# Kernel optimization log

Hardware: AMD Instinct MI355X
Metric: run time of the kernel (lower is better)

Reference implementation:

```python
import jax, jax.numpy as jnp
import numpy as np

H = 5  # hidden size == input size

def setup_inputs() -> dict:
    key = jax.random.key(0)
    ks = jax.random.split(key, 12)
    B, T = 8192, 512
    s = 1.0 / np.sqrt(H)
    x = jax.random.normal(ks[0], (B, T, H), dtype=jnp.float32)
    # LSTM params (PyTorch layout: [4H, in], gate order i,f,g,o)
    W_ih = jax.random.uniform(ks[1], (4 * H, H), jnp.float32, -s, s)
    W_hh = jax.random.uniform(ks[2], (4 * H, H), jnp.float32, -s, s)
    b_ih = jax.random.uniform(ks[3], (4 * H,), jnp.float32, -s, s)
    b_hh = jax.random.uniform(ks[4], (4 * H,), jnp.float32, -s, s)
    # MLP head 5->32->32->5 (PyTorch Linear layout: [out, in])
    W1 = jax.random.uniform(ks[5], (32, H), jnp.float32, -s, s)
    b1 = jax.random.uniform(ks[6], (32,), jnp.float32, -s, s)
    s2 = 1.0 / np.sqrt(32)
    W2 = jax.random.uniform(ks[7], (32, 32), jnp.float32, -s2, s2)
    b2 = jax.random.uniform(ks[8], (32,), jnp.float32, -s2, s2)
    W3 = jax.random.uniform(ks[9], (H, 32), jnp.float32, -s2, s2)
    b3 = jax.random.uniform(ks[10], (H,), jnp.float32, -s2, s2)
    return {"x": x, "W_ih": W_ih, "W_hh": W_hh, "b_ih": b_ih, "b_hh": b_hh,
            "W1": W1, "b1": b1, "W2": W2, "b2": b2, "W3": W3, "b3": b3}


def _lstm_last_hidden(x, W_ih, W_hh, b_ih, b_hh):
    # x: [B, T, H]. Precompute input projections for all steps: [T, B, 4H]
    xz = jnp.einsum('bth,gh->tbg', x, W_ih) + (b_ih + b_hh)
    B = x.shape[0]
    h0 = jnp.zeros((B, H), x.dtype)
    c0 = jnp.zeros((B, H), x.dtype)

    def step(carry, z_t):
        h, c = carry
        z = z_t + h @ W_hh.T  # [B, 4H]
        i = jax.nn.sigmoid(z[:, 0:H])
        f = jax.nn.sigmoid(z[:, H:2 * H])
        g = jnp.tanh(z[:, 2 * H:3 * H])
        o = jax.nn.sigmoid(z[:, 3 * H:4 * H])
        c = f * c + i * g
        h = o * jnp.tanh(c)
        return (h, c), None

    (h, _), _ = jax.lax.scan(step, (h0, c0), xz)
    return h  # [B, H]


def reference(x, W_ih, W_hh, b_ih, b_hh, W1, b1, W2, b2, W3, b3):
    h_last = _lstm_last_hidden(x, W_ih, W_hh, b_ih, b_hh)
    out = h_last + x[:, -1, :]                # residual with last input step
    out = jax.nn.relu(out @ W1.T + b1)
    out = jax.nn.relu(out @ W2.T + b2)
    out = out @ W3.T + b3
    return out
```

## Files before the change

kernel.cpp:

```cpp
#include <hip/hip_runtime.h>


#define LOG2E 1.44269504088896f

__device__ __forceinline__ float hexp2(float x) { return __builtin_amdgcn_exp2f(x); }
__device__ __forceinline__ float hrcp(float x)  { return __builtin_amdgcn_rcpf(x); }

template<int CTRL>
__device__ __forceinline__ float dpp_mov(float x) {
  int r = __builtin_amdgcn_update_dpp(0, __builtin_bit_cast(int, x),
                                      CTRL, 0xF, 0xF, true);
  return __builtin_bit_cast(float, r);
}
template<int CTRL, int BANKMASK>
__device__ __forceinline__ float dpp_merge(float old, float src) {
  int r = __builtin_amdgcn_update_dpp(__builtin_bit_cast(int, old),
                                      __builtin_bit_cast(int, src),
                                      CTRL, 0xF, BANKMASK, false);
  return __builtin_bit_cast(float, r);
}

constexpr int TT   = 512;
constexpr int HD   = 5;
constexpr int RPB  = 8;
constexpr int CHNK = 32;
constexpr int RSTR = 164;
constexpr int XOFF = RPB * RSTR;
constexpr int NCH  = TT / CHNK;

__global__ __launch_bounds__(64, 1) void lstm_mlp_kernel(
    const float* __restrict__ x,   const float* __restrict__ Wih,
    const float* __restrict__ Whh, const float* __restrict__ bih,
    const float* __restrict__ bhh, const float* __restrict__ W1,
    const float* __restrict__ b1,  const float* __restrict__ W2,
    const float* __restrict__ b2,  const float* __restrict__ W3,
    const float* __restrict__ b3,  float* __restrict__ out, int B)
{
  const int lane = threadIdx.x;
  const int grp  = lane >> 3;
  const int j    = lane & 7;
  const int jj   = (j < 5) ? j : 0;
  const int blockRow = blockIdx.x * RPB;
  const int row  = blockRow + grp;
  const bool act = (j < 5) && (row < B);

  __shared__ float xbuf[2 * XOFF];
  __shared__ float sh[RPB][5];
  __shared__ float s1[RPB][32];
  __shared__ float s2[RPB][32];

  float wih[4][5], whh[4][5], bsum[4];
#pragma unroll
  for (int G = 0; G < 4; ++G) {
    const float sc = (G == 2) ? (2.0f * LOG2E) : (-LOG2E);
#pragma unroll
    for (int k = 0; k < 5; ++k) {
      wih[G][k] = Wih[(G * 5 + jj) * 5 + k] * sc;
      whh[G][k] = Whh[(G * 5 + jj) * 5 + k] * sc;
    }
    bsum[G] = (bih[G * 5 + jj] + bhh[G * 5 + jj]) * sc;
  }

  const int rowc = (row < B) ? row : (B - 1);
  const float xlast = x[(size_t)rowc * (TT * HD) + 511 * HD + jj];

  const float4* gp[5];
  int wa[5];
#pragma unroll
  for (int i = 0; i < 5; ++i) {
    int u  = i * 64 + lane;
    int r  = u / 40;
    int o4 = u - r * 40;
    int gr = blockRow + r; if (gr >= B) gr = B - 1;
    gp[i]  = (const float4*)(x + (size_t)gr * (TT * HD)) + o4;
    wa[i]  = r * RSTR + o4 * 4;
  }

  float4 st0, st1, st2, st3, st4;
  st0 = *gp[0]; gp[0] += 40; st1 = *gp[1]; gp[1] += 40;
  st2 = *gp[2]; gp[2] += 40; st3 = *gp[3]; gp[3] += 40;
  st4 = *gp[4]; gp[4] += 40;
  *(float4*)&xbuf[wa[0]] = st0; *(float4*)&xbuf[wa[1]] = st1;
  *(float4*)&xbuf[wa[2]] = st2; *(float4*)&xbuf[wa[3]] = st3;
  *(float4*)&xbuf[wa[4]] = st4;
  st0 = *gp[0]; gp[0] += 40; st1 = *gp[1]; gp[1] += 40;
  st2 = *gp[2]; gp[2] += 40; st3 = *gp[3]; gp[3] += 40;
  st4 = *gp[4]; gp[4] += 40;

  float c = 0.0f;
  float hv0 = 0.f, hv1 = 0.f, hv2 = 0.f, hv3 = 0.f, hv4 = 0.f;

  auto step = [&](float x0, float x1, float x2, float x3, float x4) {
    float z[4];
#pragma unroll
    for (int G = 0; G < 4; ++G) {
      float a = bsum[G];
      a = fmaf(x0, wih[G][0], a);
      a = fmaf(x1, wih[G][1], a);
      a = fmaf(x2, wih[G][2], a);
      a = fmaf(x3, wih[G][3], a);
      a = fmaf(x4, wih[G][4], a);
      a = fmaf(hv0, whh[G][0], a);
      a = fmaf(hv1, whh[G][1], a);
      a = fmaf(hv2, whh[G][2], a);
      a = fmaf(hv3, whh[G][3], a);
      a = fmaf(hv4, whh[G][4], a);
      z[G] = a;
    }
    float ig = hrcp(1.0f + hexp2(z[0]));
    float fg = hrcp(1.0f + hexp2(z[1]));
    float gv = fmaf(-2.0f, hrcp(1.0f + hexp2(z[2])), 1.0f);
    float og = hrcp(1.0f + hexp2(z[3]));
    c = fmaf(fg, c, ig * gv);
    float th = fmaf(-2.0f, hrcp(1.0f + hexp2(c * (2.0f * LOG2E))), 1.0f);
    float h  = og * th;
    float q0 = dpp_mov<0x00>(h);
    float q1 = dpp_mov<0x55>(h);
    float q2 = dpp_mov<0xAA>(h);
    float q3 = dpp_mov<0xFF>(h);
    hv0 = dpp_merge<0x114, 0xA>(q0, q0);
    hv1 = dpp_merge<0x114, 0xA>(q1, q1);
    hv2 = dpp_merge<0x114, 0xA>(q2, q2);
    hv3 = dpp_merge<0x114, 0xA>(q3, q3);
    hv4 = dpp_merge<0x104, 0x5>(q0, q0);
  };

  auto step4 = [&](float4 A, float4 Bv, float4 C, float4 D, float4 E) {
    step(A.x, A.y, A.z, A.w, Bv.x);
    step(Bv.y, Bv.z, Bv.w, C.x, C.y);
    step(C.z, C.w, D.x, D.y, D.z);
    step(D.w, E.x, E.y, E.z, E.w);
  };

  auto rdg = [&](int fi, float4& A, float4& Bv, float4& C, float4& D, float4& E) {
    const float4* p = (const float4*)&xbuf[fi];
    A = p[0]; Bv = p[1]; C = p[2]; D = p[3]; E = p[4];
  };

  float4 A0, A1, A2, A3, A4;
  float4 B0, B1, B2, B3, B4;

#pragma unroll 1
  for (int ch = 0; ch < NCH; ++ch) {
    const int bo_cur  = (ch & 1) ? XOFF : 0;
    const int bo_next = XOFF - bo_cur;
    if (ch < NCH - 1) {
      *(float4*)&xbuf[wa[0] + bo_next] = st0;
      *(float4*)&xbuf[wa[1] + bo_next] = st1;
      *(float4*)&xbuf[wa[2] + bo_next] = st2;
      *(float4*)&xbuf[wa[3] + bo_next] = st3;
      *(float4*)&xbuf[wa[4] + bo_next] = st4;
    }
    if (ch < NCH - 2) {
      st0 = *gp[0]; gp[0] += 40; st1 = *gp[1]; gp[1] += 40;
      st2 = *gp[2]; gp[2] += 40; st3 = *gp[3]; gp[3] += 40;
      st4 = *gp[4]; gp[4] += 40;
    }
    const int xb = bo_cur + grp * RSTR;
    rdg(xb +   0, A0, A1, A2, A3, A4);
    rdg(xb +  20, B0, B1, B2, B3, B4);
    step4(A0, A1, A2, A3, A4); rdg(xb +  40, A0, A1, A2, A3, A4);
    step4(B0, B1, B2, B3, B4); rdg(xb +  60, B0, B1, B2, B3, B4);
    step4(A0, A1, A2, A3, A4); rdg(xb +  80, A0, A1, A2, A3, A4);
    step4(B0, B1, B2, B3, B4); rdg(xb + 100, B0, B1, B2, B3, B4);
    step4(A0, A1, A2, A3, A4); rdg(xb + 120, A0, A1, A2, A3, A4);
    step4(B0, B1, B2, B3, B4); rdg(xb + 140, B0, B1, B2, B3, B4);
    step4(A0, A1, A2, A3, A4);
    step4(B0, B1, B2, B3, B4);
  }

  if (j < 5) sh[grp][j] = hv4 * 0.0f + (hv0 * 0.0f) + 0.0f +
                          ((j == 0) ? hv0 : (j == 1) ? hv1 : (j == 2) ? hv2 :
                           (j == 3) ? hv3 : hv4) + xlast;
  float in5_0 = sh[grp][0], in5_1 = sh[grp][1], in5_2 = sh[grp][2],
        in5_3 = sh[grp][3], in5_4 = sh[grp][4];

#pragma unroll
  for (int p = 0; p < 4; ++p) {
    int m = p * 8 + j;
    float acc = b1[m];
    acc = fmaf(W1[m * 5 + 0], in5_0, acc);
    acc = fmaf(W1[m * 5 + 1], in5_1, acc);
    acc = fmaf(W1[m * 5 + 2], in5_2, acc);
    acc = fmaf(W1[m * 5 + 3], in5_3, acc);
    acc = fmaf(W1[m * 5 + 4], in5_4, acc);
    s1[grp][m] = fmaxf(acc, 0.0f);
  }
  float y1[32];
#pragma unroll
  for (int k = 0; k < 32; ++k) y1[k] = s1[grp][k];

  auto dot32 = [&](const float* W, int m, const float* y, float b) {
    float acc = b;
    const float4* w4 = (const float4*)(W + m * 32);
#pragma unroll
    for (int k4 = 0; k4 < 8; ++k4) {
      float4 w = w4[k4];
      acc = fmaf(w.x, y[k4 * 4 + 0], acc);
      acc = fmaf(w.y, y[k4 * 4 + 1], acc);
      acc = fmaf(w.z, y[k4 * 4 + 2], acc);
      acc = fmaf(w.w, y[k4 * 4 + 3], acc);
    }
    return acc;
  };

#pragma unroll
  for (int p = 0; p < 4; ++p) {
    int m = p * 8 + j;
    s2[grp][m] = fmaxf(dot32(W2, m, y1, b2[m]), 0.0f);
  }
  float y2[32];
#pragma unroll
  for (int k = 0; k < 32; ++k) y2[k] = s2[grp][k];

  if (act) out[row * HD + j] = dot32(W3, j, y2, b3[j]);
}

extern "C" void kernel_launch(void* const* d_in, const int* in_sizes, int n_in,
                              void* d_out, int out_size, void* d_ws, size_t ws_size,
                              hipStream_t stream) {
  const float* x   = (const float*)d_in[0];
  const float* Wih = (const float*)d_in[1];
  const float* Whh = (const float*)d_in[2];
  const float* bih = (const float*)d_in[3];
  const float* bhh = (const float*)d_in[4];
  const float* W1  = (const float*)d_in[5];
  const float* b1  = (const float*)d_in[6];
  const float* W2  = (const float*)d_in[7];
  const float* b2  = (const float*)d_in[8];
  const float* W3  = (const float*)d_in[9];
  const float* b3  = (const float*)d_in[10];

  int B = in_sizes[0] / (TT * HD);
  int grid = (B + RPB - 1) / RPB;
  hipLaunchKernelGGL(lstm_mlp_kernel, dim3(grid), dim3(64), 0, stream,
                     x, Wih, Whh, bih, bhh, W1, b1, W2, b2, W3, b3,
                     (float*)d_out, B);
}
```

Before: 206.7 us.

## Split LSTM into producer wave for input projections and consumer wave for recurrence

The block grows to two waves. One wave streams x into LDS and computes the input-gate projections (W_ih·x + bias) into a double-buffered LDS window. The other wave reads those precomputed projections and runs only the W_hh recurrence plus the MLP head, with block barriers handing each window across. The aim is to take the input-projection FMAs and the global-load staging off the serial recurrence wave. The cost is extra LDS traffic, per-window barriers and twice the threads per block.

```diff
diff --git a/kernel.cpp b/kernel.cpp
--- a/kernel.cpp
+++ b/kernel.cpp
@@ -27,8 +27,14 @@
 constexpr int RSTR = 164;
 constexpr int XOFF = RPB * RSTR;
 constexpr int NCH  = TT / CHNK;
-
-__global__ __launch_bounds__(64, 1) void lstm_mlp_kernel(
+constexpr int WST  = 16;
+constexpr int ZSTR = 20;
+constexpr int ZROW = RPB * ZSTR;
+constexpr int ZWIN = WST * ZROW;
+
+__global__ __attribute__((amdgpu_flat_work_group_size(128, 128),
+                          amdgpu_waves_per_eu(2, 2)))
+void lstm_mlp_kernel(
     const float* __restrict__ x,   const float* __restrict__ Wih,
     const float* __restrict__ Whh, const float* __restrict__ bih,
     const float* __restrict__ bhh, const float* __restrict__ W1,
@@ -36,70 +42,155 @@
     const float* __restrict__ b2,  const float* __restrict__ W3,
     const float* __restrict__ b3,  float* __restrict__ out, int B)
 {
-  const int lane = threadIdx.x;
+  const int tid  = threadIdx.x;
+  const int wid  = tid >> 6;
+  const int lane = tid & 63;
   const int grp  = lane >> 3;
   const int j    = lane & 7;
   const int jj   = (j < 5) ? j : 0;
   const int blockRow = blockIdx.x * RPB;
   const int row  = blockRow + grp;
-  const bool act = (j < 5) && (row < B);
-
-  __shared__ float xbuf[2 * XOFF];
-  __shared__ float sh[RPB][5];
+
+  __shared__ __align__(16) float xbuf[2 * XOFF];
+  __shared__ __align__(16) float zbuf[2 * ZWIN];
   __shared__ float s1[RPB][32];
   __shared__ float s2[RPB][32];
 
-  float wih[4][5], whh[4][5], bsum[4];
+  if (wid == 1) {
+    float wih[4][5], bsum[4];
+#pragma unroll
+    for (int G = 0; G < 4; ++G) {
+      const float sc = (G == 2) ? (2.0f * LOG2E) : (-LOG2E);
+#pragma unroll
+      for (int k = 0; k < 5; ++k)
+        wih[G][k] = Wih[(G * 5 + jj) * 5 + k] * sc;
+      bsum[G] = (bih[G * 5 + jj] + bhh[G * 5 + jj]) * sc;
+    }
+
+    const float4* gp[5];
+    int wa[5];
+#pragma unroll
+    for (int i = 0; i < 5; ++i) {
+      int u  = i * 64 + lane;
+      int r  = u / 40;
+      int o4 = u - r * 40;
+      int gr = blockRow + r; if (gr >= B) gr = B - 1;
+      gp[i]  = (const float4*)(x + (size_t)gr * (TT * HD)) + o4;
+      wa[i]  = r * RSTR + o4 * 4;
+    }
+
+    float4 st0, st1, st2, st3, st4;
+    st0 = *gp[0]; gp[0] += 40; st1 = *gp[1]; gp[1] += 40;
+    st2 = *gp[2]; gp[2] += 40; st3 = *gp[3]; gp[3] += 40;
+    st4 = *gp[4]; gp[4] += 40;
+    *(float4*)&xbuf[wa[0]] = st0; *(float4*)&xbuf[wa[1]] = st1;
+    *(float4*)&xbuf[wa[2]] = st2; *(float4*)&xbuf[wa[3]] = st3;
+    *(float4*)&xbuf[wa[4]] = st4;
+    st0 = *gp[0]; gp[0] += 40; st1 = *gp[1]; gp[1] += 40;
+    st2 = *gp[2]; gp[2] += 40; st3 = *gp[3]; gp[3] += 40;
+    st4 = *gp[4]; gp[4] += 40;
+
+    float* zb = zbuf + grp * ZSTR + jj * 4;
+
+    auto prodstep = [&](float x0, float x1, float x2, float x3, float x4,
+                        float* zp) {
+      float a[4];
+#pragma unroll
+      for (int G = 0; G < 4; ++G) {
+        float a0 = bsum[G];
+        a0 = fmaf(x0, wih[G][0], a0);
+        a0 = fmaf(x1, wih[G][1], a0);
+        a0 = fmaf(x2, wih[G][2], a0);
+        a0 = fmaf(x3, wih[G][3], a0);
+        a0 = fmaf(x4, wih[G][4], a0);
+        a[G] = a0;
+      }
+      if (j < 5) {
+        float4 v; v.x = a[0]; v.y = a[1]; v.z = a[2]; v.w = a[3];
+        *(float4*)zp = v;
+      }
+    };
+    auto prod4 = [&](float4 A, float4 Bv, float4 C, float4 D, float4 E,
+                     float* zp) {
+      prodstep(A.x, A.y, A.z, A.w, Bv.x, zp);
+      prodstep(Bv.y, Bv.z, Bv.w, C.x, C.y, zp + 1 * ZROW);
+      prodstep(C.z, C.w, D.x, D.y, D.z, zp + 2 * ZROW);
+      prodstep(D.w, E.x, E.y, E.z, E.w, zp + 3 * ZROW);
+    };
+    auto rdg = [&](int fi, float4& A, float4& Bv, float4& C, float4& D, float4& E) {
+      const float4* p = (const float4*)&xbuf[fi];
+      A = p[0]; Bv = p[1]; C = p[2]; D = p[3]; E = p[4];
+    };
+
+    float4 A0, A1, A2, A3, A4;
+    float4 B0, B1, B2, B3, B4;
+
+#pragma unroll 1
+    for (int ch = 0; ch < NCH; ++ch) {
+      const int bo_cur  = (ch & 1) ? XOFF : 0;
+      const int bo_next = XOFF - bo_cur;
+      if (ch < NCH - 1) {
+        *(float4*)&xbuf[wa[0] + bo_next] = st0;
+        *(float4*)&xbuf[wa[1] + bo_next] = st1;
+        *(float4*)&xbuf[wa[2] + bo_next] = st2;
+        *(float4*)&xbuf[wa[3] + bo_next] = st3;
+        *(float4*)&xbuf[wa[4] + bo_next] = st4;
+      }
+      if (ch < NCH - 2) {
+        st0 = *gp[0]; gp[0] += 40; st1 = *gp[1]; gp[1] += 40;
+        st2 = *gp[2]; gp[2] += 40; st3 = *gp[3]; gp[3] += 40;
+        st4 = *gp[4]; gp[4] += 40;
+      }
+      const int xb = bo_cur + grp * RSTR;
+
+      rdg(xb +  0, A0, A1, A2, A3, A4);
+      rdg(xb + 20, B0, B1, B2, B3, B4);
+      prod4(A0, A1, A2, A3, A4, zb + 0 * ZROW);
+      rdg(xb + 40, A0, A1, A2, A3, A4);
+      prod4(B0, B1, B2, B3, B4, zb + 4 * ZROW);
+      rdg(xb + 60, B0, B1, B2, B3, B4);
+      prod4(A0, A1, A2, A3, A4, zb +  8 * ZROW);
+      prod4(B0, B1, B2, B3, B4, zb + 12 * ZROW);
+      __syncthreads();
+
+      float* z1 = zb + ZWIN;
+      rdg(xb +  80, A0, A1, A2, A3, A4);
+      rdg(xb + 100, B0, B1, B2, B3, B4);
+      prod4(A0, A1, A2, A3, A4, z1 + 0 * ZROW);
+      rdg(xb + 120, A0, A1, A2, A3, A4);
+      prod4(B0, B1, B2, B3, B4, z1 + 4 * ZROW);
+      rdg(xb + 140, B0, B1, B2, B3, B4);
+      prod4(A0, A1, A2, A3, A4, z1 +  8 * ZROW);
+      prod4(B0, B1, B2, B3, B4, z1 + 12 * ZROW);
+      __syncthreads();
+    }
+    return;
+  }
+
+  float whh[4][5];
 #pragma unroll
   for (int G = 0; G < 4; ++G) {
     const float sc = (G == 2) ? (2.0f * LOG2E) : (-LOG2E);
 #pragma unroll
-    for (int k = 0; k < 5; ++k) {
-      wih[G][k] = Wih[(G * 5 + jj) * 5 + k] * sc;
+    for (int k = 0; k < 5; ++k)
       whh[G][k] = Whh[(G * 5 + jj) * 5 + k] * sc;
-    }
-    bsum[G] = (bih[G * 5 + jj] + bhh[G * 5 + jj]) * sc;
   }
 
   const int rowc = (row < B) ? row : (B - 1);
-  const float xlast = x[(size_t)rowc * (TT * HD) + 511 * HD + jj];
-
-  const float4* gp[5];
-  int wa[5];
-#pragma unroll
-  for (int i = 0; i < 5; ++i) {
-    int u  = i * 64 + lane;
-    int r  = u / 40;
-    int o4 = u - r * 40;
-    int gr = blockRow + r; if (gr >= B) gr = B - 1;
-    gp[i]  = (const float4*)(x + (size_t)gr * (TT * HD)) + o4;
-    wa[i]  = r * RSTR + o4 * 4;
-  }
-
-  float4 st0, st1, st2, st3, st4;
-  st0 = *gp[0]; gp[0] += 40; st1 = *gp[1]; gp[1] += 40;
-  st2 = *gp[2]; gp[2] += 40; st3 = *gp[3]; gp[3] += 40;
-  st4 = *gp[4]; gp[4] += 40;
-  *(float4*)&xbuf[wa[0]] = st0; *(float4*)&xbuf[wa[1]] = st1;
-  *(float4*)&xbuf[wa[2]] = st2; *(float4*)&xbuf[wa[3]] = st3;
-  *(float4*)&xbuf[wa[4]] = st4;
-  st0 = *gp[0]; gp[0] += 40; st1 = *gp[1]; gp[1] += 40;
-  st2 = *gp[2]; gp[2] += 40; st3 = *gp[3]; gp[3] += 40;
-  st4 = *gp[4]; gp[4] += 40;
+  const float xl0 = x[(size_t)rowc * (TT * HD) + 511 * HD + 0];
+  const float xl1 = x[(size_t)rowc * (TT * HD) + 511 * HD + 1];
+  const float xl2 = x[(size_t)rowc * (TT * HD) + 511 * HD + 2];
+  const float xl3 = x[(size_t)rowc * (TT * HD) + 511 * HD + 3];
+  const float xl4 = x[(size_t)rowc * (TT * HD) + 511 * HD + 4];
 
   float c = 0.0f;
   float hv0 = 0.f, hv1 = 0.f, hv2 = 0.f, hv3 = 0.f, hv4 = 0.f;
 
-  auto step = [&](float x0, float x1, float x2, float x3, float x4) {
-    float z[4];
+  auto stepz = [&](float4 zn) {
+    float z[4] = {zn.x, zn.y, zn.z, zn.w};
 #pragma unroll
     for (int G = 0; G < 4; ++G) {
-      float a = bsum[G];
-      a = fmaf(x0, wih[G][0], a);
-      a = fmaf(x1, wih[G][1], a);
-      a = fmaf(x2, wih[G][2], a);
-      a = fmaf(x3, wih[G][3], a);
-      a = fmaf(x4, wih[G][4], a);
+      float a = z[G];
       a = fmaf(hv0, whh[G][0], a);
       a = fmaf(hv1, whh[G][1], a);
       a = fmaf(hv2, whh[G][2], a);
@@ -125,55 +216,23 @@
     hv4 = dpp_merge<0x104, 0x5>(q0, q0);
   };
 
-  auto step4 = [&](float4 A, float4 Bv, float4 C, float4 D, float4 E) {
-    step(A.x, A.y, A.z, A.w, Bv.x);
-    step(Bv.y, Bv.z, Bv.w, C.x, C.y);
-    step(C.z, C.w, D.x, D.y, D.z);
-    step(D.w, E.x, E.y, E.z, E.w);
-  };
-
-  auto rdg = [&](int fi, float4& A, float4& Bv, float4& C, float4& D, float4& E) {
-    const float4* p = (const float4*)&xbuf[fi];
-    A = p[0]; Bv = p[1]; C = p[2]; D = p[3]; E = p[4];
-  };
-
-  float4 A0, A1, A2, A3, A4;
-  float4 B0, B1, B2, B3, B4;
-
 #pragma unroll 1
-  for (int ch = 0; ch < NCH; ++ch) {
-    const int bo_cur  = (ch & 1) ? XOFF : 0;
-    const int bo_next = XOFF - bo_cur;
-    if (ch < NCH - 1) {
-      *(float4*)&xbuf[wa[0] + bo_next] = st0;
-      *(float4*)&xbuf[wa[1] + bo_next] = st1;
-      *(float4*)&xbuf[wa[2] + bo_next] = st2;
-      *(float4*)&xbuf[wa[3] + bo_next] = st3;
-      *(float4*)&xbuf[wa[4] + bo_next] = st4;
-    }
-    if (ch < NCH - 2) {
-      st0 = *gp[0]; gp[0] += 40; st1 = *gp[1]; gp[1] += 40;
-      st2 = *gp[2]; gp[2] += 40; st3 = *gp[3]; gp[3] += 40;
-      st4 = *gp[4]; gp[4] += 40;
-    }
-    const int xb = bo_cur + grp * RSTR;
-    rdg(xb +   0, A0, A1, A2, A3, A4);
-    rdg(xb +  20, B0, B1, B2, B3, B4);
-    step4(A0, A1, A2, A3, A4); rdg(xb +  40, A0, A1, A2, A3, A4);
-    step4(B0, B1, B2, B3, B4); rdg(xb +  60, B0, B1, B2, B3, B4);
-    step4(A0, A1, A2, A3, A4); rdg(xb +  80, A0, A1, A2, A3, A4);
-    step4(B0, B1, B2, B3, B4); rdg(xb + 100, B0, B1, B2, B3, B4);
-    step4(A0, A1, A2, A3, A4); rdg(xb + 120, A0, A1, A2, A3, A4);
-    step4(B0, B1, B2, B3, B4); rdg(xb + 140, B0, B1, B2, B3, B4);
-    step4(A0, A1, A2, A3, A4);
-    step4(B0, B1, B2, B3, B4);
-  }
-
-  if (j < 5) sh[grp][j] = hv4 * 0.0f + (hv0 * 0.0f) + 0.0f +
-                          ((j == 0) ? hv0 : (j == 1) ? hv1 : (j == 2) ? hv2 :
-                           (j == 3) ? hv3 : hv4) + xlast;
-  float in5_0 = sh[grp][0], in5_1 = sh[grp][1], in5_2 = sh[grp][2],
-        in5_3 = sh[grp][3], in5_4 = sh[grp][4];
+  for (int w = 0; w < 2 * NCH; ++w) {
+    __syncthreads();
+    const float4* zp = (const float4*)(zbuf + (w & 1) * ZWIN) + (grp * 5 + jj);
+    float4 ZA0 = zp[0],   ZA1 = zp[40],  ZA2 = zp[80],  ZA3 = zp[120];
+    float4 ZB0 = zp[160], ZB1 = zp[200], ZB2 = zp[240], ZB3 = zp[280];
+    stepz(ZA0); stepz(ZA1); stepz(ZA2); stepz(ZA3);
+    ZA0 = zp[320]; ZA1 = zp[360]; ZA2 = zp[400]; ZA3 = zp[440];
+    stepz(ZB0); stepz(ZB1); stepz(ZB2); stepz(ZB3);
+    ZB0 = zp[480]; ZB1 = zp[520]; ZB2 = zp[560]; ZB3 = zp[600];
+    stepz(ZA0); stepz(ZA1); stepz(ZA2); stepz(ZA3);
+    stepz(ZB0); stepz(ZB1); stepz(ZB2); stepz(ZB3);
+  }
+
+  const bool act = (j < 5) && (row < B);
+  float in5_0 = hv0 + xl0, in5_1 = hv1 + xl1, in5_2 = hv2 + xl2,
+        in5_3 = hv3 + xl3, in5_4 = hv4 + xl4;
 
 #pragma unroll
   for (int p = 0; p < 4; ++p) {
@@ -233,7 +292,7 @@
 
   int B = in_sizes[0] / (TT * HD);
   int grid = (B + RPB - 1) / RPB;
-  hipLaunchKernelGGL(lstm_mlp_kernel, dim3(grid), dim3(64), 0, stream,
+  hipLaunchKernelGGL(lstm_mlp_kernel, dim3(grid), dim3(128), 0, stream,
                      x, Wih, Whh, bih, bhh, W1, b1, W2, b2, W3, b3,
                      (float*)d_out, B);
 }
```

New measurement: 215.5 us. 4.3% more time.

## Software-pipeline LSTM input projection one timestep ahead of recurrence

Applied to the files above, without the earlier changes.

Computes the input projection (bias plus W_ih·x) for step t+1 inside step t, interleaved with the exp and rcp gate math. Only the W_hh·h FMAs stay on the serial recurrence path. To support this, the chunk loop now prefetches the next chunk's first row. The residual add also moves into registers, which removes the shared-memory round trip for the final hidden state. The cost is more live registers and some scheduling complexity.

```diff
diff --git a/kernel.cpp b/kernel.cpp
--- a/kernel.cpp
+++ b/kernel.cpp
@@ -28,7 +28,9 @@
 constexpr int XOFF = RPB * RSTR;
 constexpr int NCH  = TT / CHNK;
 
-__global__ __launch_bounds__(64, 1) void lstm_mlp_kernel(
+__global__ __attribute__((amdgpu_flat_work_group_size(64, 64),
+                          amdgpu_waves_per_eu(1, 1)))
+void lstm_mlp_kernel(
     const float* __restrict__ x,   const float* __restrict__ Wih,
     const float* __restrict__ Whh, const float* __restrict__ bih,
     const float* __restrict__ bhh, const float* __restrict__ W1,
@@ -44,8 +46,7 @@
   const int row  = blockRow + grp;
   const bool act = (j < 5) && (row < B);
 
-  __shared__ float xbuf[2 * XOFF];
-  __shared__ float sh[RPB][5];
+  __shared__ __align__(16) float xbuf[2 * XOFF];
   __shared__ float s1[RPB][32];
   __shared__ float s2[RPB][32];
 
@@ -62,7 +63,11 @@
   }
 
   const int rowc = (row < B) ? row : (B - 1);
-  const float xlast = x[(size_t)rowc * (TT * HD) + 511 * HD + jj];
+  const float xl0 = x[(size_t)rowc * (TT * HD) + 511 * HD + 0];
+  const float xl1 = x[(size_t)rowc * (TT * HD) + 511 * HD + 1];
+  const float xl2 = x[(size_t)rowc * (TT * HD) + 511 * HD + 2];
+  const float xl3 = x[(size_t)rowc * (TT * HD) + 511 * HD + 3];
+  const float xl4 = x[(size_t)rowc * (TT * HD) + 511 * HD + 4];
 
   const float4* gp[5];
   int wa[5];
@@ -89,30 +94,69 @@
 
   float c = 0.0f;
   float hv0 = 0.f, hv1 = 0.f, hv2 = 0.f, hv3 = 0.f, hv4 = 0.f;
-
-  auto step = [&](float x0, float x1, float x2, float x3, float x4) {
-    float z[4];
-#pragma unroll
-    for (int G = 0; G < 4; ++G) {
-      float a = bsum[G];
-      a = fmaf(x0, wih[G][0], a);
-      a = fmaf(x1, wih[G][1], a);
-      a = fmaf(x2, wih[G][2], a);
-      a = fmaf(x3, wih[G][3], a);
-      a = fmaf(x4, wih[G][4], a);
-      a = fmaf(hv0, whh[G][0], a);
-      a = fmaf(hv1, whh[G][1], a);
-      a = fmaf(hv2, whh[G][2], a);
-      a = fmaf(hv3, whh[G][3], a);
-      a = fmaf(hv4, whh[G][4], a);
-      z[G] = a;
-    }
-    float ig = hrcp(1.0f + hexp2(z[0]));
-    float fg = hrcp(1.0f + hexp2(z[1]));
-    float gv = fmaf(-2.0f, hrcp(1.0f + hexp2(z[2])), 1.0f);
-    float og = hrcp(1.0f + hexp2(z[3]));
+  float zx0, zx1, zx2, zx3;
+
+  {
+    const float* xp = &xbuf[grp * RSTR];
+    float p0 = xp[0], p1 = xp[1], p2 = xp[2], p3 = xp[3], p4 = xp[4];
+    zx0 = bsum[0];
+    zx0 = fmaf(p0, wih[0][0], zx0); zx0 = fmaf(p1, wih[0][1], zx0);
+    zx0 = fmaf(p2, wih[0][2], zx0); zx0 = fmaf(p3, wih[0][3], zx0);
+    zx0 = fmaf(p4, wih[0][4], zx0);
+    zx1 = bsum[1];
+    zx1 = fmaf(p0, wih[1][0], zx1); zx1 = fmaf(p1, wih[1][1], zx1);
+    zx1 = fmaf(p2, wih[1][2], zx1); zx1 = fmaf(p3, wih[1][3], zx1);
+    zx1 = fmaf(p4, wih[1][4], zx1);
+    zx2 = bsum[2];
+    zx2 = fmaf(p0, wih[2][0], zx2); zx2 = fmaf(p1, wih[2][1], zx2);
+    zx2 = fmaf(p2, wih[2][2], zx2); zx2 = fmaf(p3, wih[2][3], zx2);
+    zx2 = fmaf(p4, wih[2][4], zx2);
+    zx3 = bsum[3];
+    zx3 = fmaf(p0, wih[3][0], zx3); zx3 = fmaf(p1, wih[3][1], zx3);
+    zx3 = fmaf(p2, wih[3][2], zx3); zx3 = fmaf(p3, wih[3][3], zx3);
+    zx3 = fmaf(p4, wih[3][4], zx3);
+  }
+
+  auto stepP = [&](float n0, float n1, float n2, float n3, float n4) {
+    float z0 = zx0, z1 = zx1, z2 = zx2, z3 = zx3;
+    z0 = fmaf(hv0, whh[0][0], z0); z0 = fmaf(hv1, whh[0][1], z0);
+    z0 = fmaf(hv2, whh[0][2], z0); z0 = fmaf(hv3, whh[0][3], z0);
+    z0 = fmaf(hv4, whh[0][4], z0);
+    z1 = fmaf(hv0, whh[1][0], z1); z1 = fmaf(hv1, whh[1][1], z1);
+    z1 = fmaf(hv2, whh[1][2], z1); z1 = fmaf(hv3, whh[1][3], z1);
+    z1 = fmaf(hv4, whh[1][4], z1);
+    z2 = fmaf(hv0, whh[2][0], z2); z2 = fmaf(hv1, whh[2][1], z2);
+    z2 = fmaf(hv2, whh[2][2], z2); z2 = fmaf(hv3, whh[2][3], z2);
+    z2 = fmaf(hv4, whh[2][4], z2);
+    z3 = fmaf(hv0, whh[3][0], z3); z3 = fmaf(hv1, whh[3][1], z3);
+    z3 = fmaf(hv2, whh[3][2], z3); z3 = fmaf(hv3, whh[3][3], z3);
+    z3 = fmaf(hv4, whh[3][4], z3);
+    float e0 = hexp2(z0), e1 = hexp2(z1), e2 = hexp2(z2), e3 = hexp2(z3);
+    float n_0 = bsum[0];
+    n_0 = fmaf(n0, wih[0][0], n_0); n_0 = fmaf(n1, wih[0][1], n_0);
+    n_0 = fmaf(n2, wih[0][2], n_0); n_0 = fmaf(n3, wih[0][3], n_0);
+    n_0 = fmaf(n4, wih[0][4], n_0);
+    float n_1 = bsum[1];
+    n_1 = fmaf(n0, wih[1][0], n_1); n_1 = fmaf(n1, wih[1][1], n_1);
+    n_1 = fmaf(n2, wih[1][2], n_1); n_1 = fmaf(n3, wih[1][3], n_1);
+    n_1 = fmaf(n4, wih[1][4], n_1);
+    float fg = hrcp(1.0f + e1);
+    float ig = hrcp(1.0f + e0);
+    float gr = hrcp(1.0f + e2);
+    float og = hrcp(1.0f + e3);
+    float gv = fmaf(-2.0f, gr, 1.0f);
     c = fmaf(fg, c, ig * gv);
-    float th = fmaf(-2.0f, hrcp(1.0f + hexp2(c * (2.0f * LOG2E))), 1.0f);
+    float cm = c * (2.0f * LOG2E);
+    float ec = hexp2(cm);
+    float n_2 = bsum[2];
+    n_2 = fmaf(n0, wih[2][0], n_2); n_2 = fmaf(n1, wih[2][1], n_2);
+    n_2 = fmaf(n2, wih[2][2], n_2); n_2 = fmaf(n3, wih[2][3], n_2);
+    n_2 = fmaf(n4, wih[2][4], n_2);
+    float n_3 = bsum[3];
+    n_3 = fmaf(n0, wih[3][0], n_3); n_3 = fmaf(n1, wih[3][1], n_3);
+    n_3 = fmaf(n2, wih[3][2], n_3); n_3 = fmaf(n3, wih[3][3], n_3);
+    n_3 = fmaf(n4, wih[3][4], n_3);
+    float th = fmaf(-2.0f, hrcp(1.0f + ec), 1.0f);
     float h  = og * th;
     float q0 = dpp_mov<0x00>(h);
     float q1 = dpp_mov<0x55>(h);
@@ -123,22 +167,29 @@
     hv2 = dpp_merge<0x114, 0xA>(q2, q2);
     hv3 = dpp_merge<0x114, 0xA>(q3, q3);
     hv4 = dpp_merge<0x104, 0x5>(q0, q0);
-  };
-
-  auto step4 = [&](float4 A, float4 Bv, float4 C, float4 D, float4 E) {
-    step(A.x, A.y, A.z, A.w, Bv.x);
-    step(Bv.y, Bv.z, Bv.w, C.x, C.y);
-    step(C.z, C.w, D.x, D.y, D.z);
-    step(D.w, E.x, E.y, E.z, E.w);
-  };
+    zx0 = n_0; zx1 = n_1; zx2 = n_2; zx3 = n_3;
+  };
+
+  float4 A0, A1, A2, A3, A4;
+  float4 B0, B1, B2, B3, B4;
 
   auto rdg = [&](int fi, float4& A, float4& Bv, float4& C, float4& D, float4& E) {
     const float4* p = (const float4*)&xbuf[fi];
     A = p[0]; Bv = p[1]; C = p[2]; D = p[3]; E = p[4];
   };
 
-  float4 A0, A1, A2, A3, A4;
-  float4 B0, B1, B2, B3, B4;
+  auto SUBA = [&]() {
+    stepP(A1.y, A1.z, A1.w, A2.x, A2.y);
+    stepP(A2.z, A2.w, A3.x, A3.y, A3.z);
+    stepP(A3.w, A4.x, A4.y, A4.z, A4.w);
+    stepP(B0.x, B0.y, B0.z, B0.w, B1.x);
+  };
+  auto SUBB = [&]() {
+    stepP(B1.y, B1.z, B1.w, B2.x, B2.y);
+    stepP(B2.z, B2.w, B3.x, B3.y, B3.z);
+    stepP(B3.w, B4.x, B4.y, B4.z, B4.w);
+    stepP(A0.x, A0.y, A0.z, A0.w, A1.x);
+  };
 
 #pragma unroll 1
   for (int ch = 0; ch < NCH; ++ch) {
@@ -159,21 +210,19 @@
     const int xb = bo_cur + grp * RSTR;
     rdg(xb +   0, A0, A1, A2, A3, A4);
     rdg(xb +  20, B0, B1, B2, B3, B4);
-    step4(A0, A1, A2, A3, A4); rdg(xb +  40, A0, A1, A2, A3, A4);
-    step4(B0, B1, B2, B3, B4); rdg(xb +  60, B0, B1, B2, B3, B4);
-    step4(A0, A1, A2, A3, A4); rdg(xb +  80, A0, A1, A2, A3, A4);
-    step4(B0, B1, B2, B3, B4); rdg(xb + 100, B0, B1, B2, B3, B4);
-    step4(A0, A1, A2, A3, A4); rdg(xb + 120, A0, A1, A2, A3, A4);
-    step4(B0, B1, B2, B3, B4); rdg(xb + 140, B0, B1, B2, B3, B4);
-    step4(A0, A1, A2, A3, A4);
-    step4(B0, B1, B2, B3, B4);
-  }
-
-  if (j < 5) sh[grp][j] = hv4 * 0.0f + (hv0 * 0.0f) + 0.0f +
-                          ((j == 0) ? hv0 : (j == 1) ? hv1 : (j == 2) ? hv2 :
-                           (j == 3) ? hv3 : hv4) + xlast;
-  float in5_0 = sh[grp][0], in5_1 = sh[grp][1], in5_2 = sh[grp][2],
-        in5_3 = sh[grp][3], in5_4 = sh[grp][4];
+    SUBA(); rdg(xb +  40, A0, A1, A2, A3, A4);
+    SUBB(); rdg(xb +  60, B0, B1, B2, B3, B4);
+    SUBA(); rdg(xb +  80, A0, A1, A2, A3, A4);
+    SUBB(); rdg(xb + 100, B0, B1, B2, B3, B4);
+    SUBA(); rdg(xb + 120, A0, A1, A2, A3, A4);
+    SUBB(); rdg(xb + 140, B0, B1, B2, B3, B4);
+    SUBA();
+    rdg(bo_next + grp * RSTR, A0, A1, A2, A3, A4);
+    SUBB();
+  }
+
+  float in5_0 = hv0 + xl0, in5_1 = hv1 + xl1, in5_2 = hv2 + xl2,
+        in5_3 = hv3 + xl3, in5_4 = hv4 + xl4;
 
 #pragma unroll
   for (int p = 0; p < 4; ++p) {
```

Result: no change. 204.5 us (-1.1%).
